# Optimization experiments

Hardware: AMD Instinct MI355X
Metric: run time of the kernel (lower is better)

The kernel has to match this reference:

```python
import jax, jax.numpy as jnp
import numpy as np


def log_g(x):
    # log of g(x) = x + 0.5 for x>=0, sigmoid(x) for x<0
    return jnp.where(x >= 0, jnp.log(jax.nn.relu(x) + 0.5), -jax.nn.softplus(-x))


def setup_inputs() -> dict:
    key = jax.random.key(0)
    k1, k2 = jax.random.split(key)
    B, S, D = 4, 4096, 1024
    x = jax.random.normal(k1, (B, S, D), dtype=jnp.float32)
    # nn.Linear(dim, 2*dim, bias=False) weight: [2*dim, dim], scaled like kaiming-uniform-ish
    W = jax.random.normal(k2, (2 * D, D), dtype=jnp.float32) * (1.0 / np.sqrt(D))
    return {"x": x, "W": W}


def reference(x, W):
    # x: [B, S, D], W: [2D, D] -> hidden, gate: [B, S, D]
    hg = jnp.einsum("bsd,ed->bse", x, W)
    hidden, gate = jnp.split(hg, 2, axis=-1)

    log_coeffs = -jax.nn.softplus(gate)        # log(1 - z)
    log_z = -jax.nn.softplus(-gate)            # log(z)
    log_values = log_z + log_g(hidden)

    # Heinsen associative scan in log space along seq axis
    a_star = jnp.cumsum(log_coeffs, axis=1)
    log_h0_plus_b_star = jax.lax.cumlogsumexp(log_values - a_star, axis=1)
    log_h = a_star + log_h0_plus_b_star
    out = jnp.exp(log_h)                       # [B, S, D]
    # expansion_factor == 1.0 -> to_out is Identity
    return out
```

## Files before the change

### kernel.cpp

```cpp
#include <hip/hip_runtime.h>
#include <hip/hip_bf16.h>
#include <hip/hip_fp16.h>
#include <math.h>

#define B_  4
#define S_  4096
#define D_  1024
#define M_  (B_ * S_)
#define K_  D_
#define L_  32
#define NC_ (S_ / L_)
#define NKT 16

typedef __attribute__((ext_vector_type(8))) short          bf16x8;
typedef __attribute__((ext_vector_type(8))) unsigned short u16x8;
typedef __attribute__((ext_vector_type(4))) float          f32x4;

__device__ __forceinline__ unsigned short f2bf(float f) {
    union { __hip_bfloat16 h; unsigned short u; } cv;
    cv.h = __float2bfloat16(f);
    return cv.u;
}

__device__ __forceinline__ float fast_rcp(float x) {
#if __has_builtin(__builtin_amdgcn_rcpf)
    return __builtin_amdgcn_rcpf(x);
#else
    return 1.0f / x;
#endif
}

__device__ __forceinline__ void stage16(const unsigned short* src, char* dst) {
    __builtin_amdgcn_global_load_lds(
        (const __attribute__((address_space(1))) unsigned int*)src,
        (__attribute__((address_space(3))) unsigned int*)dst, 16, 0, 0);
}

__global__ __launch_bounds__(256) void to_bf16(
    const float* __restrict__ in, unsigned short* __restrict__ out, int n8)
{
    int i = blockIdx.x * 256 + threadIdx.x;
    if (i >= n8) return;
    const float4* p = (const float4*)in + (size_t)i * 2;
    float4 a = p[0], b = p[1];
    u16x8 o;
    o[0] = f2bf(a.x); o[1] = f2bf(a.y); o[2] = f2bf(a.z); o[3] = f2bf(a.w);
    o[4] = f2bf(b.x); o[5] = f2bf(b.y); o[6] = f2bf(b.z); o[7] = f2bf(b.w);
    *(u16x8*)(out + (size_t)i * 8) = o;
}

__global__ __launch_bounds__(512, 2) void gemm_pointwise(
    const unsigned short* __restrict__ xb, const unsigned short* __restrict__ Wb,
    __half2* __restrict__ cvb)
{
    __shared__ char lds[131072];

    const int th   = threadIdx.x;
    const int lane = th & 63;
    const int wave = th >> 6;
    const int wm = wave >> 2;
    const int wn = wave & 3;

    const int wg  = blockIdx.x;
    const int swz = (wg & 7) * 64 + (wg >> 3);
    const int m0 = (swz >> 3) * 256;
    const int d0 = (swz & 7) * 128;

    f32x4 acc[8][4];
#pragma unroll
    for (int i = 0; i < 8; ++i)
#pragma unroll
        for (int j = 0; j < 4; ++j)
            acc[i][j] = (f32x4){0.f, 0.f, 0.f, 0.f};

    const int srow = th >> 2;
    const int scol = (((th & 3) ^ ((th >> 3) & 3)) * 8);
    const unsigned short* srcA  = xb + (size_t)(m0 + srow)       * K_ + scol;
    const unsigned short* srcA2 = xb + (size_t)(m0 + 128 + srow) * K_ + scol;
    const unsigned short* srcBh = Wb + (size_t)(d0 + srow)       * K_ + scol;
    const unsigned short* srcBg = Wb + (size_t)(D_ + d0 + srow)  * K_ + scol;
    char* const wuo = lds + wave * 1024;

    const int lr  = lane & 15;
    const int lkb = (((lane >> 4) ^ ((lr >> 1) & 3)) * 16);
    const int aoffb = (wm * 128 + lr) * 64 + lkb;
    const int boffb = 32768 + (wn * 32 + lr) * 64 + lkb;

    bf16x8 Aa[4], Ab[4], Ba[4], Bb[4];

#define BAR()  asm volatile("s_barrier" ::: "memory")
#define LGK0() asm volatile("s_waitcnt lgkmcnt(0)" ::: "memory")
#define VM0()  asm volatile("s_waitcnt vmcnt(0)" ::: "memory")

#define CLUSTER(base, AF, BF) do {                                        \
    __builtin_amdgcn_s_setprio(1);                                        \
    _Pragma("unroll")                                                     \
    for (int i_ = 0; i_ < 4; ++i_)                                        \
        _Pragma("unroll")                                                 \
        for (int j_ = 0; j_ < 4; ++j_)                                    \
            acc[(base) + i_][j_] = __builtin_amdgcn_mfma_f32_16x16x32_bf16(\
                AF[i_], BF[j_], acc[(base) + i_][j_], 0, 0, 0);           \
    __builtin_amdgcn_s_setprio(0);                                        \
  } while (0)

    stage16(srcA,       wuo + 0);
    stage16(srcA2,      wuo + 8192);
    stage16(srcA  + 32, wuo + 16384);
    stage16(srcA2 + 32, wuo + 24576);
    stage16(srcBh,      wuo + 32768);
    stage16(srcBg,      wuo + 40960);
    stage16(srcBh + 32, wuo + 49152);
    stage16(srcBg + 32, wuo + 57344);
    VM0();
    BAR();
    {
        const char* bc = lds;
#pragma unroll
        for (int i = 0; i < 4; ++i)
            Aa[i] = *(const bf16x8*)(bc + aoffb + i * 1024);
#pragma unroll
        for (int j = 0; j < 2; ++j) {
            Ba[j]     = *(const bf16x8*)(bc + boffb + j * 1024);
            Ba[j + 2] = *(const bf16x8*)(bc + boffb + 8192 + j * 1024);
        }
    }

#pragma unroll 1
    for (int t = 0; t < NKT; ++t) {
        const char* bc  = lds + (t & 1) * 65536;
        char*       bn  = wuo + ((t + 1) & 1) * 65536;
        const char* bnr = lds + ((t + 1) & 1) * 65536;
        const int kof = (t + 1) * 64;
        const bool pre = (t < NKT - 1);

#pragma unroll
        for (int i = 0; i < 4; ++i)
            Ab[i] = *(const bf16x8*)(bc + aoffb + 4096 + i * 1024);
        if (pre) {
            stage16(srcA  + kof,      bn + 0);
            stage16(srcA2 + kof,      bn + 8192);
            stage16(srcA  + kof + 32, bn + 16384);
            stage16(srcA2 + kof + 32, bn + 24576);
        }
        BAR(); LGK0();
        CLUSTER(0, Aa, Ba);
        BAR();

#pragma unroll
        for (int i = 0; i < 4; ++i)
            Aa[i] = *(const bf16x8*)(bc + aoffb + 16384 + i * 1024);
#pragma unroll
        for (int j = 0; j < 2; ++j) {
            Bb[j]     = *(const bf16x8*)(bc + boffb + 16384 + j * 1024);
            Bb[j + 2] = *(const bf16x8*)(bc + boffb + 16384 + 8192 + j * 1024);
        }
        if (pre) {
            stage16(srcBh + kof,      bn + 32768);
            stage16(srcBg + kof,      bn + 40960);
            stage16(srcBh + kof + 32, bn + 49152);
            stage16(srcBg + kof + 32, bn + 57344);
        }
        BAR(); LGK0();
        CLUSTER(4, Ab, Ba);
        BAR();

#pragma unroll
        for (int i = 0; i < 4; ++i)
            Ab[i] = *(const bf16x8*)(bc + aoffb + 4096 + 16384 + i * 1024);
        BAR(); LGK0();
        CLUSTER(0, Aa, Bb);
        BAR();

        VM0();
        BAR();
        if (pre) {
#pragma unroll
            for (int i = 0; i < 4; ++i)
                Aa[i] = *(const bf16x8*)(bnr + aoffb + i * 1024);
#pragma unroll
            for (int j = 0; j < 2; ++j) {
                Ba[j]     = *(const bf16x8*)(bnr + boffb + j * 1024);
                Ba[j + 2] = *(const bf16x8*)(bnr + boffb + 8192 + j * 1024);
            }
        }
        CLUSTER(4, Ab, Bb);
    }
#undef CLUSTER
#undef BAR
#undef LGK0
#undef VM0

#pragma unroll
    for (int mi = 0; mi < 8; ++mi)
#pragma unroll
        for (int nj = 0; nj < 2; ++nj)
#pragma unroll
            for (int r = 0; r < 4; ++r) {
                int m = m0 + wm * 128 + mi * 16 + ((lane >> 4) << 2) + r;
                int d = d0 + wn * 32 + nj * 16 + lr;
                float h = acc[mi][nj][r];
                float g = acc[mi][nj + 2][r];
                float eg  = __expf(g);
                float c   = fast_rcp(1.0f + eg);
                float z   = eg * c;
                float enh = __expf(-h);
                float sh  = fast_rcp(1.0f + enh);
                float gh  = (h >= 0.0f) ? (h + 0.5f) : sh;
                float v   = z * gh;
                cvb[(size_t)m * D_ + d] = __floats2half2_rn(c, v);
            }
}

__global__ __launch_bounds__(256) void chunk_reduce(
    const unsigned int* __restrict__ cvw,
    float2* __restrict__ CVagg)
{
    const int d = (blockIdx.x * 256 + threadIdx.x) * 2;
    const int c = blockIdx.y;
    const int b = blockIdx.z;
    size_t base = ((size_t)(b * S_ + c * L_)) * D_ + d;
    float C0 = 1.f, V0 = 0.f, C1 = 1.f, V1 = 0.f;
    for (int s = 0; s < L_; ++s) {
        uint2 u = *(const uint2*)(cvw + base + (size_t)s * D_);
        float2 p0 = __half22float2(*(const __half2*)&u.x);
        float2 p1 = __half22float2(*(const __half2*)&u.y);
        V0 = fmaf(p0.x, V0, p0.y);  C0 *= p0.x;
        V1 = fmaf(p1.x, V1, p1.y);  C1 *= p1.x;
    }
    size_t o = ((size_t)b * NC_ + c) * D_ + d;
    float4 st = {C0, V0, C1, V1};
    *(float4*)(CVagg + o) = st;
}

__global__ __launch_bounds__(256) void chunk_scan(
    const float2* __restrict__ CVagg, float* __restrict__ P)
{
    const int d = blockIdx.x * 256 + threadIdx.x;
    const int b = blockIdx.z;
    float h = 0.0f;
    for (int c = 0; c < NC_; ++c) {
        size_t o = ((size_t)b * NC_ + c) * D_ + d;
        P[o] = h;
        float2 cv = CVagg[o];
        h = fmaf(cv.x, h, cv.y);
    }
}

__global__ __launch_bounds__(256) void chunk_apply(
    const unsigned int* __restrict__ cvw, const float* __restrict__ P,
    float* __restrict__ out)
{
    const int d = (blockIdx.x * 256 + threadIdx.x) * 2;
    const int c = blockIdx.y;
    const int b = blockIdx.z;
    size_t base = ((size_t)(b * S_ + c * L_)) * D_ + d;
    float2 h2 = *(const float2*)(P + ((size_t)b * NC_ + c) * D_ + d);
    float h0 = h2.x, h1 = h2.y;
    for (int s = 0; s < L_; ++s) {
        uint2 u = *(const uint2*)(cvw + base + (size_t)s * D_);
        float2 p0 = __half22float2(*(const __half2*)&u.x);
        float2 p1 = __half22float2(*(const __half2*)&u.y);
        h0 = fmaf(p0.x, h0, p0.y);
        h1 = fmaf(p1.x, h1, p1.y);
        float2 o2 = {h0, h1};
        *(float2*)(out + base + (size_t)s * D_) = o2;
    }
}

extern "C" void kernel_launch(void* const* d_in, const int* in_sizes, int n_in,
                              void* d_out, int out_size, void* d_ws, size_t ws_size,
                              hipStream_t stream) {
    const float* x = (const float*)d_in[0];
    const float* W = (const float*)d_in[1];
    float* out = (float*)d_out;

    float2* CVagg = (float2*)d_ws;
    float*  P     = (float*)(CVagg + (size_t)B_ * NC_ * D_);
    __half2* cvb  = (__half2*)(P + (size_t)B_ * NC_ * D_);
    unsigned short* xb = (unsigned short*)(cvb + (size_t)M_ * D_);
    unsigned short* Wb = xb + (size_t)M_ * K_;

    const int nx8 = M_ * K_ / 8;
    const int nw8 = 2 * D_ * K_ / 8;
    to_bf16<<<(nx8 + 255) / 256, 256, 0, stream>>>(x, xb, nx8);
    to_bf16<<<(nw8 + 255) / 256, 256, 0, stream>>>(W, Wb, nw8);

    gemm_pointwise<<<512, 512, 0, stream>>>(xb, Wb, cvb);

    dim3 g2(D_ / 512, NC_, B_);
    chunk_reduce<<<g2, 256, 0, stream>>>((const unsigned int*)cvb, CVagg);

    dim3 g3(D_ / 256, 1, B_);
    chunk_scan<<<g3, 256, 0, stream>>>(CVagg, P);

    chunk_apply<<<g2, 256, 0, stream>>>((const unsigned int*)cvb, P, out);
}
```

Before: 135.2 us.

## Switch GEMM mainloop to 4-buffer, 3-deep prefetch with K-tile of 32

Replaces the double-buffered 64-wide K tile with a 4-slot ring of 32-wide K tiles. Global-to-LDS loads are issued three tiles ahead, with partial vmcnt waits instead of a full drain each iteration. The goal is to hide global memory latency behind MFMA work. In exchange it doubles the number of iterations and barriers per tile, and the vmcnt counts have to match the number of stage instructions issued.

Result: slower. 138.1 us (+2.1%).

```diff
diff --git a/kernel.cpp b/kernel.cpp
--- a/kernel.cpp
+++ b/kernel.cpp
@@ -10,7 +10,7 @@
 #define K_  D_
 #define L_  32
 #define NC_ (S_ / L_)
-#define NKT 16
+#define NKT 32
 
 typedef __attribute__((ext_vector_type(8))) short          bf16x8;
 typedef __attribute__((ext_vector_type(8))) unsigned short u16x8;
@@ -84,111 +84,78 @@
     const int lr  = lane & 15;
     const int lkb = (((lane >> 4) ^ ((lr >> 1) & 3)) * 16);
     const int aoffb = (wm * 128 + lr) * 64 + lkb;
-    const int boffb = 32768 + (wn * 32 + lr) * 64 + lkb;
-
-    bf16x8 Aa[4], Ab[4], Ba[4], Bb[4];
+    const int boffb = 16384 + (wn * 32 + lr) * 64 + lkb;
+
+    bf16x8 Af[4], Bf[4];
 
 #define BAR()  asm volatile("s_barrier" ::: "memory")
 #define LGK0() asm volatile("s_waitcnt lgkmcnt(0)" ::: "memory")
-#define VM0()  asm volatile("s_waitcnt vmcnt(0)" ::: "memory")
-
-#define CLUSTER(base, AF, BF) do {                                        \
+#define VMW(n) asm volatile("s_waitcnt vmcnt(" #n ")" ::: "memory")
+
+#define STAGE_A(tt) do { const int ko_ = (tt) * 32;                      \
+    char* d_ = wuo + ((tt) & 3) * 32768;                                 \
+    stage16(srcA  + ko_, d_);                                            \
+    stage16(srcA2 + ko_, d_ + 8192); } while (0)
+#define STAGE_B(tt) do { const int ko_ = (tt) * 32;                      \
+    char* d_ = wuo + ((tt) & 3) * 32768;                                 \
+    stage16(srcBh + ko_, d_ + 16384);                                    \
+    stage16(srcBg + ko_, d_ + 24576); } while (0)
+
+#define CLUSTER(base) do {                                                \
     __builtin_amdgcn_s_setprio(1);                                        \
     _Pragma("unroll")                                                     \
     for (int i_ = 0; i_ < 4; ++i_)                                        \
         _Pragma("unroll")                                                 \
         for (int j_ = 0; j_ < 4; ++j_)                                    \
             acc[(base) + i_][j_] = __builtin_amdgcn_mfma_f32_16x16x32_bf16(\
-                AF[i_], BF[j_], acc[(base) + i_][j_], 0, 0, 0);           \
+                Af[i_], Bf[j_], acc[(base) + i_][j_], 0, 0, 0);           \
     __builtin_amdgcn_s_setprio(0);                                        \
   } while (0)
 
-    stage16(srcA,       wuo + 0);
-    stage16(srcA2,      wuo + 8192);
-    stage16(srcA  + 32, wuo + 16384);
-    stage16(srcA2 + 32, wuo + 24576);
-    stage16(srcBh,      wuo + 32768);
-    stage16(srcBg,      wuo + 40960);
-    stage16(srcBh + 32, wuo + 49152);
-    stage16(srcBg + 32, wuo + 57344);
-    VM0();
+#define TILEBODY(T, PRE, WAITOP) do {                                     \
+    const char* bc_ = lds + ((T) & 3) * 32768;                            \
+    _Pragma("unroll")                                                     \
+    for (int i_ = 0; i_ < 4; ++i_)                                        \
+        Af[i_] = *(const bf16x8*)(bc_ + aoffb + i_ * 1024);               \
+    _Pragma("unroll")                                                     \
+    for (int j_ = 0; j_ < 2; ++j_) {                                      \
+        Bf[j_]     = *(const bf16x8*)(bc_ + boffb + j_ * 1024);           \
+        Bf[j_ + 2] = *(const bf16x8*)(bc_ + boffb + 8192 + j_ * 1024);    \
+    }                                                                     \
+    if (PRE) { STAGE_A((T) + 3); }                                        \
+    BAR(); LGK0();                                                        \
+    CLUSTER(0);                                                           \
+    BAR();                                                                \
+    _Pragma("unroll")                                                     \
+    for (int i_ = 0; i_ < 4; ++i_)                                        \
+        Af[i_] = *(const bf16x8*)(bc_ + aoffb + 4096 + i_ * 1024);        \
+    if (PRE) { STAGE_B((T) + 3); }                                        \
+    BAR(); LGK0();                                                        \
+    CLUSTER(4);                                                           \
+    WAITOP;                                                               \
+    BAR();                                                                \
+  } while (0)
+
+    STAGE_A(0); STAGE_B(0);
+    STAGE_A(1); STAGE_B(1);
+    STAGE_A(2); STAGE_B(2);
+    VMW(8);
     BAR();
-    {
-        const char* bc = lds;
-#pragma unroll
-        for (int i = 0; i < 4; ++i)
-            Aa[i] = *(const bf16x8*)(bc + aoffb + i * 1024);
-#pragma unroll
-        for (int j = 0; j < 2; ++j) {
-            Ba[j]     = *(const bf16x8*)(bc + boffb + j * 1024);
-            Ba[j + 2] = *(const bf16x8*)(bc + boffb + 8192 + j * 1024);
-        }
-    }
 
 #pragma unroll 1
-    for (int t = 0; t < NKT; ++t) {
-        const char* bc  = lds + (t & 1) * 65536;
-        char*       bn  = wuo + ((t + 1) & 1) * 65536;
-        const char* bnr = lds + ((t + 1) & 1) * 65536;
-        const int kof = (t + 1) * 64;
-        const bool pre = (t < NKT - 1);
-
-#pragma unroll
-        for (int i = 0; i < 4; ++i)
-            Ab[i] = *(const bf16x8*)(bc + aoffb + 4096 + i * 1024);
-        if (pre) {
-            stage16(srcA  + kof,      bn + 0);
-            stage16(srcA2 + kof,      bn + 8192);
-            stage16(srcA  + kof + 32, bn + 16384);
-            stage16(srcA2 + kof + 32, bn + 24576);
-        }
-        BAR(); LGK0();
-        CLUSTER(0, Aa, Ba);
-        BAR();
-
-#pragma unroll
-        for (int i = 0; i < 4; ++i)
-            Aa[i] = *(const bf16x8*)(bc + aoffb + 16384 + i * 1024);
-#pragma unroll
-        for (int j = 0; j < 2; ++j) {
-            Bb[j]     = *(const bf16x8*)(bc + boffb + 16384 + j * 1024);
-            Bb[j + 2] = *(const bf16x8*)(bc + boffb + 16384 + 8192 + j * 1024);
-        }
-        if (pre) {
-            stage16(srcBh + kof,      bn + 32768);
-            stage16(srcBg + kof,      bn + 40960);
-            stage16(srcBh + kof + 32, bn + 49152);
-            stage16(srcBg + kof + 32, bn + 57344);
-        }
-        BAR(); LGK0();
-        CLUSTER(4, Ab, Ba);
-        BAR();
-
-#pragma unroll
-        for (int i = 0; i < 4; ++i)
-            Ab[i] = *(const bf16x8*)(bc + aoffb + 4096 + 16384 + i * 1024);
-        BAR(); LGK0();
-        CLUSTER(0, Aa, Bb);
-        BAR();
-
-        VM0();
-        BAR();
-        if (pre) {
-#pragma unroll
-            for (int i = 0; i < 4; ++i)
-                Aa[i] = *(const bf16x8*)(bnr + aoffb + i * 1024);
-#pragma unroll
-            for (int j = 0; j < 2; ++j) {
-                Ba[j]     = *(const bf16x8*)(bnr + boffb + j * 1024);
-                Ba[j + 2] = *(const bf16x8*)(bnr + boffb + 8192 + j * 1024);
-            }
-        }
-        CLUSTER(4, Ab, Bb);
-    }
+    for (int t = 0; t < NKT - 3; ++t)
+        TILEBODY(t, 1, VMW(8));
+    TILEBODY(NKT - 3, 0, VMW(4));
+    TILEBODY(NKT - 2, 0, VMW(0));
+    TILEBODY(NKT - 1, 0, (void)0);
+
+#undef TILEBODY
 #undef CLUSTER
+#undef STAGE_A
+#undef STAGE_B
 #undef BAR
 #undef LGK0
-#undef VM0
+#undef VMW
 
 #pragma unroll
     for (int mi = 0; mi < 8; ++mi)
```

## Fuse chunk reduction into GEMM epilogue via cross-lane shuffles

Applied to the files above, without the earlier changes.

Computes each 32-row chunk's aggregate (product of coefficients and scanned value) directly in the GEMM epilogue, using wave shuffles across the MFMA row groups, and writes CVagg there. This removes the separate chunk_reduce kernel, which re-read the whole fp16 cv buffer. It also aggregates from fp32 values instead of fp16-rounded ones, which slightly changes numerics relative to the apply pass. It adds shuffle and ALU work to the GEMM epilogue.

New measurement: 127.5 us. 1.06x faster.

```diff
diff --git a/kernel.cpp b/kernel.cpp
--- a/kernel.cpp
+++ b/kernel.cpp
@@ -51,7 +51,7 @@
 
 __global__ __launch_bounds__(512, 2) void gemm_pointwise(
     const unsigned short* __restrict__ xb, const unsigned short* __restrict__ Wb,
-    __half2* __restrict__ cvb)
+    __half2* __restrict__ cvb, float2* __restrict__ CVagg)
 {
     __shared__ char lds[131072];
 
@@ -81,8 +81,9 @@
     const unsigned short* srcBg = Wb + (size_t)(D_ + d0 + srow)  * K_ + scol;
     char* const wuo = lds + wave * 1024;
 
-    const int lr  = lane & 15;
-    const int lkb = (((lane >> 4) ^ ((lr >> 1) & 3)) * 16);
+    const int lr = lane & 15;
+    const int lq = lane >> 4;
+    const int lkb = ((lq ^ ((lr >> 1) & 3)) * 16);
     const int aoffb = (wm * 128 + lr) * 64 + lkb;
     const int boffb = 32768 + (wn * 32 + lr) * 64 + lkb;
 
@@ -191,45 +192,54 @@
 #undef VM0
 
 #pragma unroll
-    for (int mi = 0; mi < 8; ++mi)
-#pragma unroll
-        for (int nj = 0; nj < 2; ++nj)
-#pragma unroll
-            for (int r = 0; r < 4; ++r) {
-                int m = m0 + wm * 128 + mi * 16 + ((lane >> 4) << 2) + r;
-                int d = d0 + wn * 32 + nj * 16 + lr;
-                float h = acc[mi][nj][r];
-                float g = acc[mi][nj + 2][r];
-                float eg  = __expf(g);
-                float c   = fast_rcp(1.0f + eg);
-                float z   = eg * c;
-                float enh = __expf(-h);
-                float sh  = fast_rcp(1.0f + enh);
-                float gh  = (h >= 0.0f) ? (h + 0.5f) : sh;
-                float v   = z * gh;
-                cvb[(size_t)m * D_ + d] = __floats2half2_rn(c, v);
+    for (int mp = 0; mp < 4; ++mp) {
+        float C16[2][2], V16[2][2];
+#pragma unroll
+        for (int hf = 0; hf < 2; ++hf) {
+            const int mi = mp * 2 + hf;
+#pragma unroll
+            for (int nj = 0; nj < 2; ++nj) {
+                float C4 = 1.0f, V4 = 0.0f;
+                const int d = d0 + wn * 32 + nj * 16 + lr;
+#pragma unroll
+                for (int r = 0; r < 4; ++r) {
+                    int m = m0 + wm * 128 + mi * 16 + lq * 4 + r;
+                    float h = acc[mi][nj][r];
+                    float g = acc[mi][nj + 2][r];
+                    float eg  = __expf(g);
+                    float c   = fast_rcp(1.0f + eg);
+                    float z   = eg * c;
+                    float enh = __expf(-h);
+                    float sh  = fast_rcp(1.0f + enh);
+                    float gh  = (h >= 0.0f) ? (h + 0.5f) : sh;
+                    float v   = z * gh;
+                    cvb[(size_t)m * D_ + d] = __floats2half2_rn(c, v);
+                    V4 = fmaf(c, V4, v);
+                    C4 *= c;
+                }
+                float Ca = __shfl_xor(C4, 16), Va = __shfl_xor(V4, 16);
+                float Clo = (lq & 1) ? Ca : C4, Vlo = (lq & 1) ? Va : V4;
+                float Chi = (lq & 1) ? C4 : Ca, Vhi = (lq & 1) ? V4 : Va;
+                float C2 = Clo * Chi, V2 = fmaf(Chi, Vlo, Vhi);
+                float Cb = __shfl_xor(C2, 32), Vb = __shfl_xor(V2, 32);
+                float Cl2 = (lq & 2) ? Cb : C2, Vl2 = (lq & 2) ? Vb : V2;
+                float Ch2 = (lq & 2) ? C2 : Cb, Vh2 = (lq & 2) ? V2 : Vb;
+                C16[hf][nj] = Cl2 * Ch2;
+                V16[hf][nj] = fmaf(Ch2, Vl2, Vh2);
             }
-}
-
-__global__ __launch_bounds__(256) void chunk_reduce(
-    const unsigned int* __restrict__ cvw,
-    float2* __restrict__ CVagg)
-{
-    const int d = (blockIdx.x * 256 + threadIdx.x) * 2;
-    const int c = blockIdx.y;
-    const int b = blockIdx.z;
-    size_t base = ((size_t)(b * S_ + c * L_)) * D_ + d;
-    float C0 = 1.f, V0 = 0.f, C1 = 1.f, V1 = 0.f;
-    for (int s = 0; s < L_; ++s) {
-        uint2 u = *(const uint2*)(cvw + base + (size_t)s * D_);
-        float2 p0 = __half22float2(*(const __half2*)&u.x);
-        float2 p1 = __half22float2(*(const __half2*)&u.y);
-        V0 = fmaf(p0.x, V0, p0.y);  C0 *= p0.x;
-        V1 = fmaf(p1.x, V1, p1.y);  C1 *= p1.x;
-    }
-    size_t o = ((size_t)b * NC_ + c) * D_ + d;
-    float4 st = {C0, V0, C1, V1};
-    *(float4*)(CVagg + o) = st;
+        }
+        if (lq == 0) {
+            const int chunkg = (m0 + wm * 128 + mp * 32) >> 5;
+#pragma unroll
+            for (int nj = 0; nj < 2; ++nj) {
+                float C32 = C16[0][nj] * C16[1][nj];
+                float V32 = fmaf(C16[1][nj], V16[0][nj], V16[1][nj]);
+                const int d = d0 + wn * 32 + nj * 16 + lr;
+                float2 st; st.x = C32; st.y = V32;
+                CVagg[(size_t)chunkg * D_ + d] = st;
+            }
+        }
+    }
 }
 
 __global__ __launch_bounds__(256) void chunk_scan(
@@ -285,13 +295,11 @@
     to_bf16<<<(nx8 + 255) / 256, 256, 0, stream>>>(x, xb, nx8);
     to_bf16<<<(nw8 + 255) / 256, 256, 0, stream>>>(W, Wb, nw8);
 
-    gemm_pointwise<<<512, 512, 0, stream>>>(xb, Wb, cvb);
-
-    dim3 g2(D_ / 512, NC_, B_);
-    chunk_reduce<<<g2, 256, 0, stream>>>((const unsigned int*)cvb, CVagg);
+    gemm_pointwise<<<512, 512, 0, stream>>>(xb, Wb, cvb, CVagg);
 
     dim3 g3(D_ / 256, 1, B_);
     chunk_scan<<<g3, 256, 0, stream>>>(CVagg, P);
 
+    dim3 g2(D_ / 512, NC_, B_);
     chunk_apply<<<g2, 256, 0, stream>>>((const unsigned int*)cvb, P, out);
 }
```
